# Performance work log

Hardware: AMD Instinct MI355X
Metric: run time of the kernel (lower is better)

## Reference

```python
import jax, jax.numpy as jnp
import numpy as np

B, TE, TD, D = 32, 2048, 64, 1024

def setup_inputs() -> dict:
    key = jax.random.key(0)
    k1, k2, k3, k4, k5 = jax.random.split(key, 5)
    return {
        "encoder_outputs": jax.random.normal(k1, (B, TE, D), dtype=jnp.float32),
        "decoder_outputs": jax.random.normal(k2, (B, TD, D), dtype=jnp.float32),
        "W_a": jax.random.normal(k3, (D, D), dtype=jnp.float32) * (1.0 / np.sqrt(D)),
        "U_a": jax.random.normal(k4, (D, D), dtype=jnp.float32) * (1.0 / np.sqrt(D)),
        "V_a": jax.random.normal(k5, (D, 1), dtype=jnp.float32) * (1.0 / np.sqrt(D)),
    }

def reference(encoder_outputs, decoder_outputs, W_a, U_a, V_a):
    # Bahdanau additive attention over encoder positions, query = last decoder step.
    dec_last = decoder_outputs[:, -1, :]                      # [B, D]
    enc_W = jnp.einsum('bte,ef->btf', encoder_outputs, W_a)   # [B, Te, D]
    dec_U = jnp.einsum('bd,df->bf', dec_last, U_a)            # [B, D] (broadcast over Te instead of tile)
    tanh_out = jnp.tanh(enc_W + dec_U[:, None, :])            # [B, Te, D]
    scores = jnp.einsum('btf,fo->bt', tanh_out, V_a[:, 0:1])  # [B, Te] (squeeze of [B,Te,1])
    weights = jax.nn.softmax(scores, axis=1)                  # [B, Te]
    context = jnp.einsum('bte,bt->be', encoder_outputs, weights)  # [B, D]
    return context, weights[..., None]
```

## Files before the change

### kernel.cpp

```cpp
#include <hip/hip_runtime.h>
#include <stdint.h>

#define GLOBAL_AS __attribute__((address_space(1)))
#define LDS_AS    __attribute__((address_space(3)))

typedef __attribute__((ext_vector_type(8))) __bf16 bf16x8;
typedef __attribute__((ext_vector_type(4))) float  f32x4;

__device__ __forceinline__ uint16_t f2b(float f) {
  uint32_t u = __float_as_uint(f);
  u += 0x7fffu + ((u >> 16) & 1u);
  return (uint16_t)(u >> 16);
}
__device__ __forceinline__ float b2f_lo(uint32_t p) { return __uint_as_float(p << 16); }
__device__ __forceinline__ float b2f_hi(uint32_t p) { return __uint_as_float(p & 0xffff0000u); }

__device__ __forceinline__ float tanh_fast(float x) {
  float e = __expf(2.0f * x);
  return 1.0f - 2.0f / (e + 1.0f);
}

#define ASYNC16(gptr, lptr)                                                     \
  __builtin_amdgcn_global_load_lds((GLOBAL_AS void*)(uintptr_t)(gptr),          \
                                   (LDS_AS void*)(lptr), 16, 0, 0)

__global__ __launch_bounds__(256) void convert_enc(const float4* __restrict__ in,
                                                   uint4* __restrict__ out) {
  int i = blockIdx.x * 256 + threadIdx.x;
  float4 a = in[2 * i], b = in[2 * i + 1];
  uint4 o;
  o.x = (uint32_t)f2b(a.x) | ((uint32_t)f2b(a.y) << 16);
  o.y = (uint32_t)f2b(a.z) | ((uint32_t)f2b(a.w) << 16);
  o.z = (uint32_t)f2b(b.x) | ((uint32_t)f2b(b.y) << 16);
  o.w = (uint32_t)f2b(b.z) | ((uint32_t)f2b(b.w) << 16);
  out[i] = o;
}

__global__ __launch_bounds__(256) void convert_WT(const float* __restrict__ W,
                                                  uint16_t* __restrict__ WT) {
  __shared__ float tile[64][65];
  int k0 = (blockIdx.x & 15) * 64;
  int n0 = (blockIdx.x >> 4) * 64;
  #pragma unroll
  for (int it = 0; it < 16; ++it) {
    int idx = it * 256 + threadIdx.x;
    int kr = idx >> 6, nc = idx & 63;
    tile[kr][nc] = W[(size_t)(k0 + kr) * 1024 + n0 + nc];
  }
  __syncthreads();
  #pragma unroll
  for (int it = 0; it < 16; ++it) {
    int idx = it * 256 + threadIdx.x;
    int nr = idx >> 6, kc = idx & 63;
    WT[(size_t)(n0 + nr) * 1024 + k0 + kc] = f2b(tile[kc][nr]);
  }
}

__global__ __launch_bounds__(256) void compute_u(const float* __restrict__ dec,
                                                 const float4* __restrict__ U4,
                                                 float* __restrict__ u) {
  int b = blockIdx.x >> 3, dseg = blockIdx.x & 7;
  __shared__ float sdec[128];
  if (threadIdx.x < 128)
    sdec[threadIdx.x] = dec[(size_t)b * 64 * 1024 + 63 * 1024 + dseg * 128 + threadIdx.x];
  __syncthreads();
  float4 a = {0.f, 0.f, 0.f, 0.f};
  const float4* Ub = U4 + (size_t)dseg * 128 * 256 + threadIdx.x;
  #pragma unroll 4
  for (int d = 0; d < 128; ++d) {
    float4 w = Ub[(size_t)d * 256];
    float s = sdec[d];
    a.x = fmaf(s, w.x, a.x);
    a.y = fmaf(s, w.y, a.y);
    a.z = fmaf(s, w.z, a.z);
    a.w = fmaf(s, w.w, a.w);
  }
  float* up = u + b * 1024 + threadIdx.x * 4;
  atomicAdd(up + 0, a.x);
  atomicAdd(up + 1, a.y);
  atomicAdd(up + 2, a.z);
  atomicAdd(up + 3, a.w);
}

__global__ __launch_bounds__(256) void gemm_score(const uint16_t* __restrict__ A,
                                                  const uint16_t* __restrict__ BT,
                                                  const float* __restrict__ u,
                                                  const float* __restrict__ v,
                                                  float* __restrict__ spart) {
  __shared__ __bf16 sA[128 * 32];
  __shared__ __bf16 sB[128 * 32];
  __shared__ float sred[128];

  int bx = blockIdx.x;
  int g = bx >> 6, r = bx & 63;
  int mtile = g * 8 + (r & 7);
  int ntile = r >> 3;

  int tid = threadIdx.x;
  int lane = tid & 63;
  int wid  = tid >> 6;
  int wm = (wid & 1) * 64;
  int wn = (wid >> 1) * 64;
  int quad = lane >> 4, nib = lane & 15;

  f32x4 acc[4][4];
  #pragma unroll
  for (int i = 0; i < 4; ++i)
    #pragma unroll
    for (int j = 0; j < 4; ++j) acc[i][j] = (f32x4){0.f, 0.f, 0.f, 0.f};

  const int rowA = mtile * 128;
  const int rowB = ntile * 128;
  const int c0 = tid, c1 = tid + 256;
  const int r0 = ((c0 >> 6) << 4) | (c0 & 15), k0c = ((c0 >> 4) & 3) * 8;
  const int r1 = ((c1 >> 6) << 4) | (c1 & 15), k1c = ((c1 >> 4) & 3) * 8;

  for (int k0 = 0; k0 < 1024; k0 += 32) {
    __syncthreads();
    ASYNC16(A  + (size_t)(rowA + r0) * 1024 + k0 + k0c, sA + c0 * 8);
    ASYNC16(A  + (size_t)(rowA + r1) * 1024 + k0 + k1c, sA + c1 * 8);
    ASYNC16(BT + (size_t)(rowB + r0) * 1024 + k0 + k0c, sB + c0 * 8);
    ASYNC16(BT + (size_t)(rowB + r1) * 1024 + k0 + k1c, sB + c1 * 8);
    __syncthreads();

    bf16x8 af[4], bf[4];
    #pragma unroll
    for (int i = 0; i < 4; ++i)
      af[i] = *(const bf16x8*)(sA + ((wm >> 4) + i) * 512 + lane * 8);
    #pragma unroll
    for (int j = 0; j < 4; ++j)
      bf[j] = *(const bf16x8*)(sB + ((wn >> 4) + j) * 512 + lane * 8);

    #pragma unroll
    for (int i = 0; i < 4; ++i)
      #pragma unroll
      for (int j = 0; j < 4; ++j)
        acc[i][j] = __builtin_amdgcn_mfma_f32_16x16x32_bf16(af[i], bf[j], acc[i][j], 0, 0, 0);
  }

  int b = rowA >> 11;
  float vv[4], uu[4];
  #pragma unroll
  for (int j = 0; j < 4; ++j) {
    int col = ntile * 128 + wn + j * 16 + nib;
    vv[j] = v[col];
    uu[j] = u[b * 1024 + col];
  }
  float sloc[4][4];
  #pragma unroll
  for (int i = 0; i < 4; ++i) {
    #pragma unroll
    for (int reg = 0; reg < 4; ++reg) {
      float s = 0.f;
      #pragma unroll
      for (int j = 0; j < 4; ++j) s += vv[j] * tanh_fast(acc[i][j][reg] + uu[j]);
      s += __shfl_xor(s, 1);
      s += __shfl_xor(s, 2);
      s += __shfl_xor(s, 4);
      s += __shfl_xor(s, 8);
      sloc[i][reg] = s;
    }
  }
  if (wid < 2) {
    if (nib == 0) {
      #pragma unroll
      for (int i = 0; i < 4; ++i)
        #pragma unroll
        for (int reg = 0; reg < 4; ++reg)
          sred[wm + i * 16 + quad * 4 + reg] = sloc[i][reg];
    }
  }
  __syncthreads();
  if (wid >= 2 && nib == 0) {
    float* outp = spart + (size_t)ntile * 65536 + rowA;
    #pragma unroll
    for (int i = 0; i < 4; ++i) {
      int rloc = wm + i * 16 + quad * 4;
      float4 sv;
      #pragma unroll
      for (int reg = 0; reg < 4; ++reg)
        ((float*)&sv)[reg] = sloc[i][reg] + sred[rloc + reg];
      *(float4*)(outp + rloc) = sv;
    }
  }
}

__global__ __launch_bounds__(256) void softmax_k(const float* __restrict__ spart,
                                                 float* __restrict__ wout) {
  int b = blockIdx.x, tid = threadIdx.x;
  __shared__ float red[4];
  float sv[8];
  float mx = -1e30f;
  #pragma unroll
  for (int i = 0; i < 8; ++i) {
    int idx = b * 2048 + i * 256 + tid;
    float s = 0.f;
    #pragma unroll
    for (int j = 0; j < 8; ++j) s += spart[j * 65536 + idx];
    sv[i] = s;
    mx = fmaxf(mx, s);
  }
  #pragma unroll
  for (int off = 1; off < 64; off <<= 1) mx = fmaxf(mx, __shfl_xor(mx, off));
  if ((tid & 63) == 0) red[tid >> 6] = mx;
  __syncthreads();
  mx = fmaxf(fmaxf(red[0], red[1]), fmaxf(red[2], red[3]));
  __syncthreads();
  float sum = 0.f;
  #pragma unroll
  for (int i = 0; i < 8; ++i) {
    sv[i] = __expf(sv[i] - mx);
    sum += sv[i];
  }
  #pragma unroll
  for (int off = 1; off < 64; off <<= 1) sum += __shfl_xor(sum, off);
  if ((tid & 63) == 0) red[tid >> 6] = sum;
  __syncthreads();
  float inv = 1.0f / (red[0] + red[1] + red[2] + red[3]);
  #pragma unroll
  for (int i = 0; i < 8; ++i) wout[b * 2048 + i * 256 + tid] = sv[i] * inv;
}

__global__ __launch_bounds__(256) void context_k(const uint16_t* __restrict__ encA,
                                                 const float* __restrict__ w,
                                                 float* __restrict__ ctx) {
  int b = blockIdx.x >> 4, ch = blockIdx.x & 15;
  int t0 = ch * 128;
  __shared__ float lw[128];
  if (threadIdx.x < 128) lw[threadIdx.x] = w[b * 2048 + t0 + threadIdx.x];
  __syncthreads();
  int e0 = threadIdx.x * 4;
  float a0 = 0.f, a1 = 0.f, a2 = 0.f, a3 = 0.f;
  const uint16_t* base = encA + (size_t)b * 2048 * 1024 + (size_t)t0 * 1024 + e0;
  #pragma unroll 4
  for (int t = 0; t < 128; ++t) {
    uint2 p = *(const uint2*)(base + (size_t)t * 1024);
    float wt = lw[t];
    a0 = fmaf(wt, b2f_lo(p.x), a0);
    a1 = fmaf(wt, b2f_hi(p.x), a1);
    a2 = fmaf(wt, b2f_lo(p.y), a2);
    a3 = fmaf(wt, b2f_hi(p.y), a3);
  }
  atomicAdd(&ctx[b * 1024 + e0 + 0], a0);
  atomicAdd(&ctx[b * 1024 + e0 + 1], a1);
  atomicAdd(&ctx[b * 1024 + e0 + 2], a2);
  atomicAdd(&ctx[b * 1024 + e0 + 3], a3);
}

extern "C" void kernel_launch(void* const* d_in, const int* in_sizes, int n_in,
                              void* d_out, int out_size, void* d_ws, size_t ws_size,
                              hipStream_t stream) {
  const float* enc = (const float*)d_in[0];
  const float* dec = (const float*)d_in[1];
  const float* Wa  = (const float*)d_in[2];
  const float* Ua  = (const float*)d_in[3];
  const float* Va  = (const float*)d_in[4];

  float* out = (float*)d_out;
  float* ctx = out;
  float* wts = out + 32 * 1024;

  char* ws = (char*)d_ws;
  uint16_t* encA  = (uint16_t*)ws;
  uint16_t* WT    = (uint16_t*)(ws + 134217728);
  float*    ub    = (float*)  (ws + 136314880);
  float*    spart = (float*)  (ws + 136445952);

  hipMemsetAsync(ctx, 0, 32 * 1024 * sizeof(float), stream);
  hipMemsetAsync(ub, 0, 32 * 1024 * sizeof(float), stream);

  convert_enc<<<32768, 256, 0, stream>>>((const float4*)enc, (uint4*)encA);
  convert_WT<<<256, 256, 0, stream>>>(Wa, WT);
  compute_u<<<256, 256, 0, stream>>>(dec, (const float4*)Ua, ub);
  gemm_score<<<4096, 256, 0, stream>>>(encA, WT, ub, Va, spart);
  softmax_k<<<32, 256, 0, stream>>>(spart, wts);
  context_k<<<512, 256, 0, stream>>>(encA, wts, ctx);
}
```

Measured before the change: 698.2 us.

## Software-pipeline GEMM mainloop with register prefetch and double-buffered LDS

```diff
diff --git a/kernel.cpp b/kernel.cpp
--- a/kernel.cpp
+++ b/kernel.cpp
@@ -1,8 +1,5 @@
 #include <hip/hip_runtime.h>
 #include <stdint.h>
-
-#define GLOBAL_AS __attribute__((address_space(1)))
-#define LDS_AS    __attribute__((address_space(3)))
 
 typedef __attribute__((ext_vector_type(8))) __bf16 bf16x8;
 typedef __attribute__((ext_vector_type(4))) float  f32x4;
@@ -20,9 +17,9 @@
   return 1.0f - 2.0f / (e + 1.0f);
 }
 
-#define ASYNC16(gptr, lptr)                                                     \
-  __builtin_amdgcn_global_load_lds((GLOBAL_AS void*)(uintptr_t)(gptr),          \
-                                   (LDS_AS void*)(lptr), 16, 0, 0)
+__device__ __forceinline__ void barrier_lgkm() {
+  asm volatile("s_waitcnt lgkmcnt(0)\n\ts_barrier" ::: "memory");
+}
 
 __global__ __launch_bounds__(256) void convert_enc(const float4* __restrict__ in,
                                                    uint4* __restrict__ out) {
@@ -82,13 +79,12 @@
   atomicAdd(up + 3, a.w);
 }
 
-__global__ __launch_bounds__(256) void gemm_score(const uint16_t* __restrict__ A,
-                                                  const uint16_t* __restrict__ BT,
-                                                  const float* __restrict__ u,
-                                                  const float* __restrict__ v,
-                                                  float* __restrict__ spart) {
-  __shared__ __bf16 sA[128 * 32];
-  __shared__ __bf16 sB[128 * 32];
+__global__ __launch_bounds__(256, 3) void gemm_score(const uint16_t* __restrict__ A,
+                                                     const uint16_t* __restrict__ BT,
+                                                     const float* __restrict__ u,
+                                                     const float* __restrict__ v,
+                                                     float* __restrict__ spart) {
+  __shared__ uint4 sAB[2][1024];
   __shared__ float sred[128];
 
   int bx = blockIdx.x;
@@ -112,30 +108,47 @@
   const int rowA = mtile * 128;
   const int rowB = ntile * 128;
   const int c0 = tid, c1 = tid + 256;
-  const int r0 = ((c0 >> 6) << 4) | (c0 & 15), k0c = ((c0 >> 4) & 3) * 8;
-  const int r1 = ((c1 >> 6) << 4) | (c1 & 15), k1c = ((c1 >> 4) & 3) * 8;
-
-  for (int k0 = 0; k0 < 1024; k0 += 32) {
-    __syncthreads();
-    ASYNC16(A  + (size_t)(rowA + r0) * 1024 + k0 + k0c, sA + c0 * 8);
-    ASYNC16(A  + (size_t)(rowA + r1) * 1024 + k0 + k1c, sA + c1 * 8);
-    ASYNC16(BT + (size_t)(rowB + r0) * 1024 + k0 + k0c, sB + c0 * 8);
-    ASYNC16(BT + (size_t)(rowB + r1) * 1024 + k0 + k1c, sB + c1 * 8);
-    __syncthreads();
-
+  const uint4* pA0 = (const uint4*)(A  + (size_t)(rowA + (c0 >> 2)) * 1024 + (c0 & 3) * 8);
+  const uint4* pA1 = (const uint4*)(A  + (size_t)(rowA + (c1 >> 2)) * 1024 + (c1 & 3) * 8);
+  const uint4* pB0 = (const uint4*)(BT + (size_t)(rowB + (c0 >> 2)) * 1024 + (c0 & 3) * 8);
+  const uint4* pB1 = (const uint4*)(BT + (size_t)(rowB + (c1 >> 2)) * 1024 + (c1 & 3) * 8);
+  const int s0 = ((c0 >> 6) << 6) | ((c0 & 3) << 4) | ((c0 >> 2) & 15);
+  const int s1 = ((c1 >> 6) << 6) | ((c1 & 3) << 4) | ((c1 >> 2) & 15);
+
+  uint4 ra0[2], ra1[2], rb0[2], rb1[2];
+
+  ra0[0] = pA0[0]; ra1[0] = pA1[0]; rb0[0] = pB0[0]; rb1[0] = pB1[0];
+  ra0[1] = pA0[4]; ra1[1] = pA1[4]; rb0[1] = pB0[4]; rb1[1] = pB1[4];
+  sAB[0][s0] = ra0[0]; sAB[0][s1] = ra1[0];
+  sAB[0][512 + s0] = rb0[0]; sAB[0][512 + s1] = rb1[0];
+  barrier_lgkm();
+
+  #pragma unroll 2
+  for (int k = 0; k < 32; ++k) {
+    const int cur = k & 1, nxt = cur ^ 1;
+    if (k < 30) {
+      ra0[cur] = pA0[(k + 2) * 4]; ra1[cur] = pA1[(k + 2) * 4];
+      rb0[cur] = pB0[(k + 2) * 4]; rb1[cur] = pB1[(k + 2) * 4];
+    }
     bf16x8 af[4], bf[4];
     #pragma unroll
     for (int i = 0; i < 4; ++i)
-      af[i] = *(const bf16x8*)(sA + ((wm >> 4) + i) * 512 + lane * 8);
+      af[i] = *(const bf16x8*)&sAB[cur][((wm >> 4) + i) * 64 + lane];
     #pragma unroll
     for (int j = 0; j < 4; ++j)
-      bf[j] = *(const bf16x8*)(sB + ((wn >> 4) + j) * 512 + lane * 8);
+      bf[j] = *(const bf16x8*)&sAB[cur][512 + ((wn >> 4) + j) * 64 + lane];
 
     #pragma unroll
     for (int i = 0; i < 4; ++i)
       #pragma unroll
       for (int j = 0; j < 4; ++j)
         acc[i][j] = __builtin_amdgcn_mfma_f32_16x16x32_bf16(af[i], bf[j], acc[i][j], 0, 0, 0);
+
+    if (k < 31) {
+      sAB[nxt][s0] = ra0[nxt]; sAB[nxt][s1] = ra1[nxt];
+      sAB[nxt][512 + s0] = rb0[nxt]; sAB[nxt][512 + s1] = rb1[nxt];
+    }
+    barrier_lgkm();
   }
 
   int b = rowA >> 11;
```

Measured after the change: 1.181 ms. +69.1%, slower.
